# Performance work log

Hardware: AMD Instinct MI355X
Metric: run time of the kernel (lower is better)

The kernel has to match this reference:

```python
import jax, jax.numpy as jnp
import numpy as np

B, T, F, H = 64, 512, 512, 512  # batch, steps, features, hidden (both directions)


def setup_inputs() -> dict:
    key = jax.random.key(0)
    ks = jax.random.split(key, 7)
    s_in = 1.0 / np.sqrt(F)
    s_h = 1.0 / np.sqrt(H)
    return {
        "x": jax.random.normal(ks[0], (B, T, F), dtype=jnp.float32),
        "Wf": jax.random.normal(ks[1], (F, H), dtype=jnp.float32) * s_in,  # fw kernel
        "Uf": jax.random.normal(ks[2], (H, H), dtype=jnp.float32) * s_h,   # fw recurrent
        "bf": jnp.zeros((H,), dtype=jnp.float32),
        "Wb": jax.random.normal(ks[3], (F, H), dtype=jnp.float32) * s_in,  # bw kernel
        "Ub": jax.random.normal(ks[4], (H, H), dtype=jnp.float32) * s_h,   # bw recurrent
        "bb": jnp.zeros((H,), dtype=jnp.float32),
    }


def _rnn_scan(xs_tbf, W, U, b):
    # SimpleRNNCell: h' = tanh(x @ W + h @ U + b); xs_tbf: [T, B, F]
    h0 = jnp.zeros((xs_tbf.shape[1], U.shape[0]), dtype=xs_tbf.dtype)
    xw = jnp.einsum('tbf,fh->tbh', xs_tbf, W) + b  # precompute input projection

    def step(h, xw_t):
        h_new = jnp.tanh(xw_t + h @ U)
        return h_new, h_new

    _, ys = jax.lax.scan(step, h0, xw)  # ys: [T, B, H]
    return ys


def reference(x, Wf, Uf, bf, Wb, Ub, bb):
    xt = jnp.transpose(x, (1, 0, 2))              # [T, B, F]
    fw = _rnn_scan(xt, Wf, Uf, bf)                # time order
    bw = _rnn_scan(xt[::-1], Wb, Ub, bb)          # reverse-time order (NOT flipped back,
                                                  # matching the TF code which concats
                                                  # bw outputs in loop order)
    out = jnp.concatenate([fw, bw], axis=-1)      # [T, B, 2H]
    return jnp.transpose(out, (1, 0, 2))          # [B, T, 2H]
```

## Files before the change

### kernel.cpp

```cpp
#include <hip/hip_runtime.h>
#include <hip/hip_bf16.h>


using bf16 = __hip_bfloat16;
typedef __attribute__((ext_vector_type(8))) short short8;
typedef __attribute__((ext_vector_type(4))) float float4v;

#define T_STEPS 512

#define HB_OFF  1024
#define WS_ZERO_BYTES (HB_OFF + 2 * 131072 * 2)

__device__ __forceinline__ unsigned short f2bf(float f) {
    unsigned u = __builtin_bit_cast(unsigned, f);
    u = (u + 0x7fffu + ((u >> 16) & 1u)) >> 16;
    return (unsigned short)u;
}
__device__ __forceinline__ float bf2f(unsigned short s) {
    unsigned u = ((unsigned)s) << 16;
    return __builtin_bit_cast(float, u);
}

__global__ __launch_bounds__(256) void gemm_xw(
    const float* __restrict__ x,
    const float* __restrict__ Wf, const float* __restrict__ bf_,
    const float* __restrict__ Wb, const float* __restrict__ bb_,
    float* __restrict__ out)
{
    int bid = blockIdx.x;
    int dir = bid >> 12;
    int r   = bid & 4095;
    int i   = r & 63;
    int G   = r >> 6;
    int mt  = G * 8 + (i & 7);
    int nt  = i >> 3;
    const float* W    = dir ? Wb  : Wf;
    const float* bias = dir ? bb_ : bf_;

    __shared__ __align__(16) bf16 Xl[64][40];
    __shared__ __align__(16) bf16 Wt[64][40];

    int tid  = threadIdx.x;
    int wave = tid >> 6;
    int lane = tid & 63;
    int lm   = lane & 15;
    int quad = lane >> 4;

    float4v acc[4];
    #pragma unroll
    for (int q = 0; q < 4; ++q) acc[q] = (float4v){0.f, 0.f, 0.f, 0.f};

    int row0 = mt * 64;
    int srow = tid >> 2;
    int sk8  = (tid & 3) * 8;
    int wrow = tid >> 3;
    int wn8  = (tid & 7) * 8;

    for (int kt = 0; kt < 16; ++kt) {
        int k0 = kt * 32;
        const float* xp = x + (size_t)(row0 + srow) * 512 + k0 + sk8;
        float4v xa = *(const float4v*)xp;
        float4v xb = *(const float4v*)(xp + 4);
        union { short8 v; bf16 e[8]; } ux;
        ux.e[0] = __float2bfloat16(xa.x); ux.e[1] = __float2bfloat16(xa.y);
        ux.e[2] = __float2bfloat16(xa.z); ux.e[3] = __float2bfloat16(xa.w);
        ux.e[4] = __float2bfloat16(xb.x); ux.e[5] = __float2bfloat16(xb.y);
        ux.e[6] = __float2bfloat16(xb.z); ux.e[7] = __float2bfloat16(xb.w);
        *(short8*)&Xl[srow][sk8] = ux.v;
        const float* wp = W + (size_t)(k0 + wrow) * 512 + nt * 64 + wn8;
        float4v wa = *(const float4v*)wp;
        float4v wb = *(const float4v*)(wp + 4);
        Wt[wn8 + 0][wrow] = __float2bfloat16(wa.x);
        Wt[wn8 + 1][wrow] = __float2bfloat16(wa.y);
        Wt[wn8 + 2][wrow] = __float2bfloat16(wa.z);
        Wt[wn8 + 3][wrow] = __float2bfloat16(wa.w);
        Wt[wn8 + 4][wrow] = __float2bfloat16(wb.x);
        Wt[wn8 + 5][wrow] = __float2bfloat16(wb.y);
        Wt[wn8 + 6][wrow] = __float2bfloat16(wb.z);
        Wt[wn8 + 7][wrow] = __float2bfloat16(wb.w);
        __syncthreads();

        short8 a = *(const short8*)&Xl[wave * 16 + lm][quad * 8];
        #pragma unroll
        for (int n4 = 0; n4 < 4; ++n4) {
            short8 bfr = *(const short8*)&Wt[n4 * 16 + lm][quad * 8];
            acc[n4] = __builtin_amdgcn_mfma_f32_16x16x32_bf16(a, bfr, acc[n4], 0, 0, 0);
        }
        __syncthreads();
    }

    #pragma unroll
    for (int n4 = 0; n4 < 4; ++n4) {
        int ncol = nt * 64 + n4 * 16 + lm;
        float bv = bias[ncol];
        #pragma unroll
        for (int rr = 0; rr < 4; ++rr) {
            int m = wave * 16 + quad * 4 + rr;
            int gg = row0 + m;
            int b = gg >> 9;
            int t = gg & 511;
            int tp = dir ? (511 - t) : t;
            out[((size_t)b * T_STEPS + tp) * 1024 + dir * 512 + ncol] = acc[n4][rr] + bv;
        }
    }
}

__global__ __launch_bounds__(128, 1) void rnn_rec(
    const float* __restrict__ Uf, const float* __restrict__ Ub,
    float* __restrict__ out, unsigned char* __restrict__ ws)
{
    unsigned* flags = (unsigned*)ws;
    unsigned short* Hbuf = (unsigned short*)(ws + HB_OFF);

    int bid = blockIdx.x;
    int g   = bid & 31;
    int m   = bid >> 5;
    int n0  = g * 16;
    int m0  = m * 16;

    int tid  = threadIdx.x;
    int dir  = tid >> 6;
    int lane = tid & 63;
    int lm   = lane & 15;
    int quad = lane >> 4;

    const float* U = dir ? Ub : Uf;

    short8 Bh[16], Bl[16];
    #pragma unroll
    for (int kt = 0; kt < 16; ++kt) {
        union { short8 v; unsigned short e[8]; } h, l;
        #pragma unroll
        for (int j = 0; j < 8; ++j) {
            int k = kt * 32 + quad * 8 + j;
            float f = U[(size_t)k * 512 + n0 + lm];
            unsigned short hi = f2bf(f);
            h.e[j] = hi;
            l.e[j] = f2bf(f - bf2f(hi));
        }
        Bh[kt] = h.v;
        Bl[kt] = l.v;
    }

    unsigned* fbase = flags + (dir * 4 + m) * 32;
    unsigned short* base = Hbuf + (size_t)dir * 131072;
    float* od = out + (size_t)dir * 512;

    int rowb = m0 + quad * 4;
    int col  = n0 + lm;
    const size_t arow = (size_t)(m0 + lm) * 512;

    float xw[4];
    #pragma unroll
    for (int r = 0; r < 4; ++r)
        xw[r] = od[((size_t)(rowb + r) * T_STEPS + 0) * 1024 + col];

    for (int t = 0; t < T_STEPS; ++t) {
        int ph = t & 1;
        unsigned short* Hh = base + (size_t)ph * 65536;
        unsigned short* Hl = Hh + 32768;
        unsigned short* Wh = base + (size_t)(ph ^ 1) * 65536;
        unsigned short* Wl = Wh + 32768;

        if (t) {
            unsigned tgt = (unsigned)t;
            unsigned f;
            do {
                f = (lane < 32)
                  ? __hip_atomic_load(fbase + lane, __ATOMIC_RELAXED,
                                      __HIP_MEMORY_SCOPE_AGENT)
                  : tgt;
            } while (!__all(f >= tgt));
        }

        float4v aa = {0,0,0,0}, ab = {0,0,0,0}, ac = {0,0,0,0};
        #pragma unroll
        for (int kt = 0; kt < 16; ++kt) {
            int ko = kt * 32 + quad * 8;
            unsigned long long* pa = (unsigned long long*)(Hh + arow + ko);
            unsigned long long* pl = (unsigned long long*)(Hl + arow + ko);
            union { unsigned long long q[2]; short8 s; } ua, ul;
            ua.q[0] = __hip_atomic_load(pa,     __ATOMIC_RELAXED, __HIP_MEMORY_SCOPE_AGENT);
            ua.q[1] = __hip_atomic_load(pa + 1, __ATOMIC_RELAXED, __HIP_MEMORY_SCOPE_AGENT);
            ul.q[0] = __hip_atomic_load(pl,     __ATOMIC_RELAXED, __HIP_MEMORY_SCOPE_AGENT);
            ul.q[1] = __hip_atomic_load(pl + 1, __ATOMIC_RELAXED, __HIP_MEMORY_SCOPE_AGENT);
            aa = __builtin_amdgcn_mfma_f32_16x16x32_bf16(ua.s, Bh[kt], aa, 0, 0, 0);
            ab = __builtin_amdgcn_mfma_f32_16x16x32_bf16(ul.s, Bh[kt], ab, 0, 0, 0);
            ac = __builtin_amdgcn_mfma_f32_16x16x32_bf16(ua.s, Bl[kt], ac, 0, 0, 0);
        }

        float4v s = aa + ab + ac;
        float hv[4];
        #pragma unroll
        for (int r = 0; r < 4; ++r)
            hv[r] = tanhf(s[r] + xw[r]);

        #pragma unroll
        for (int r = 0; r < 4; ++r) {
            unsigned short hb = f2bf(hv[r]);
            unsigned short lb = f2bf(hv[r] - bf2f(hb));
            unsigned myw = (unsigned)hb | ((unsigned)lb << 16);
            unsigned p = (unsigned)__shfl_xor((int)myw, 1);
            if (!(lane & 1)) {
                unsigned hiw = (myw & 0xFFFFu) | (p << 16);
                unsigned low = (myw >> 16) | (p & 0xFFFF0000u);
                size_t off = (size_t)(rowb + r) * 512 + col;
                __hip_atomic_store((unsigned*)(Wh + off), hiw,
                                   __ATOMIC_RELAXED, __HIP_MEMORY_SCOPE_AGENT);
                __hip_atomic_store((unsigned*)(Wl + off), low,
                                   __ATOMIC_RELAXED, __HIP_MEMORY_SCOPE_AGENT);
            }
        }

        asm volatile("s_waitcnt vmcnt(0)" ::: "memory");
        if (lane == 0)
            __hip_atomic_store(fbase + g, (unsigned)(t + 1),
                               __ATOMIC_RELAXED, __HIP_MEMORY_SCOPE_AGENT);

        #pragma unroll
        for (int r = 0; r < 4; ++r)
            od[((size_t)(rowb + r) * T_STEPS + t) * 1024 + col] = hv[r];

        int tn = (t + 1 < T_STEPS) ? (t + 1) : t;
        #pragma unroll
        for (int r = 0; r < 4; ++r)
            xw[r] = od[((size_t)(rowb + r) * T_STEPS + tn) * 1024 + col];
    }
}

extern "C" void kernel_launch(void* const* d_in, const int* in_sizes, int n_in,
                              void* d_out, int out_size, void* d_ws, size_t ws_size,
                              hipStream_t stream) {
    const float* x   = (const float*)d_in[0];
    const float* Wf  = (const float*)d_in[1];
    const float* Uf  = (const float*)d_in[2];
    const float* bf_ = (const float*)d_in[3];
    const float* Wb  = (const float*)d_in[4];
    const float* Ub  = (const float*)d_in[5];
    const float* bb_ = (const float*)d_in[6];
    float* out = (float*)d_out;

    hipMemsetAsync(d_ws, 0, WS_ZERO_BYTES, stream);
    hipLaunchKernelGGL(gemm_xw, dim3(8192), dim3(256), 0, stream,
                       x, Wf, bf_, Wb, bb_, out);
    hipLaunchKernelGGL(rnn_rec, dim3(128), dim3(128), 0, stream,
                       Uf, Ub, out, (unsigned char*)d_ws);
}
```

Before: 4.253 ms.

## Co-locate recurrence groups per XCD and pipeline hidden-state loads with epoch flags

The recurrent kernel now assigns both waves of a block to the same direction and batch tile, so each group's 16 blocks are strided so they may land on one XCD. A startup barrier records each block's XCC id to decide whether a fast path is safe. The fast path polls flags with sc0 loads, which appear intended to stay coherent within an XCD, and software-pipelines the hidden-state loads with explicit vmcnt waits; otherwise it falls back to agent-scope atomics. Epoch-tagged flags, bumped by the GEMM kernel, avoid re-zeroing the large hidden buffer each call, the low part of U moves to LDS to save registers, and correctness now depends on the hardware's block placement and cache behaviour.

```diff
diff --git a/kernel.cpp b/kernel.cpp
--- a/kernel.cpp
+++ b/kernel.cpp
@@ -8,8 +8,8 @@
 
 #define T_STEPS 512
 
-#define HB_OFF  1024
-#define WS_ZERO_BYTES (HB_OFF + 2 * 131072 * 2)
+#define HB_OFF  2048
+#define WS_HDR_ZERO 1664
 
 __device__ __forceinline__ unsigned short f2bf(float f) {
     unsigned u = __builtin_bit_cast(unsigned, f);
@@ -25,9 +25,13 @@
     const float* __restrict__ x,
     const float* __restrict__ Wf, const float* __restrict__ bf_,
     const float* __restrict__ Wb, const float* __restrict__ bb_,
-    float* __restrict__ out)
+    float* __restrict__ out, unsigned char* __restrict__ ws)
 {
     int bid = blockIdx.x;
+    if (bid == 0 && threadIdx.x == 0) {
+        __hip_atomic_fetch_add((unsigned*)(ws + 1664), 1u,
+                               __ATOMIC_RELAXED, __HIP_MEMORY_SCOPE_AGENT);
+    }
     int dir = bid >> 12;
     int r   = bid & 4095;
     int i   = r & 63;
@@ -95,8 +99,8 @@
         float bv = bias[ncol];
         #pragma unroll
         for (int rr = 0; rr < 4; ++rr) {
-            int m = wave * 16 + quad * 4 + rr;
-            int gg = row0 + m;
+            int mm = wave * 16 + quad * 4 + rr;
+            int gg = row0 + mm;
             int b = gg >> 9;
             int t = gg & 511;
             int tp = dir ? (511 - t) : t;
@@ -110,39 +114,56 @@
     float* __restrict__ out, unsigned char* __restrict__ ws)
 {
     unsigned* flags = (unsigned*)ws;
+    unsigned* xcct  = (unsigned*)(ws + 1024);
+    unsigned* barc  = (unsigned*)(ws + 1536);
     unsigned short* Hbuf = (unsigned short*)(ws + HB_OFF);
 
     int bid = blockIdx.x;
-    int g   = bid & 31;
-    int m   = bid >> 5;
-    int n0  = g * 16;
-    int m0  = m * 16;
+    int grp = bid & 7;
+    int dir = grp >> 2;
+    int m   = grp & 3;
+    int j   = bid >> 3;
 
     int tid  = threadIdx.x;
-    int dir  = tid >> 6;
+    int wv   = tid >> 6;
     int lane = tid & 63;
     int lm   = lane & 15;
     int quad = lane >> 4;
+    int g    = j * 2 + wv;
+    int n0   = g * 16;
+    int m0   = m * 16;
+
+    unsigned ep = __hip_atomic_load((unsigned*)(ws + 1664),
+                                    __ATOMIC_RELAXED, __HIP_MEMORY_SCOPE_AGENT);
+    unsigned ebase = ep << 10;
+
+    if (tid == 0) {
+        unsigned xid = __builtin_amdgcn_s_getreg(20 | (0 << 6) | (31 << 11)) & 0xffu;
+        __hip_atomic_store(xcct + bid, xid | 0x100u,
+                           __ATOMIC_RELAXED, __HIP_MEMORY_SCOPE_AGENT);
+        __hip_atomic_fetch_add(barc, 1u, __ATOMIC_RELAXED, __HIP_MEMORY_SCOPE_AGENT);
+    }
 
     const float* U = dir ? Ub : Uf;
 
-    short8 Bh[16], Bl[16];
+    __shared__ __align__(16) short8 BlLds[2][16][64];
+    short8 Bh[16];
     #pragma unroll
     for (int kt = 0; kt < 16; ++kt) {
         union { short8 v; unsigned short e[8]; } h, l;
         #pragma unroll
-        for (int j = 0; j < 8; ++j) {
-            int k = kt * 32 + quad * 8 + j;
+        for (int jj = 0; jj < 8; ++jj) {
+            int k = kt * 32 + quad * 8 + jj;
             float f = U[(size_t)k * 512 + n0 + lm];
             unsigned short hi = f2bf(f);
-            h.e[j] = hi;
-            l.e[j] = f2bf(f - bf2f(hi));
+            h.e[jj] = hi;
+            l.e[jj] = f2bf(f - bf2f(hi));
         }
         Bh[kt] = h.v;
-        Bl[kt] = l.v;
-    }
-
-    unsigned* fbase = flags + (dir * 4 + m) * 32;
+        BlLds[wv][kt][lane] = l.v;
+    }
+
+    unsigned* fbase = flags + grp * 32;
     unsigned short* base = Hbuf + (size_t)dir * 131072;
     float* od = out + (size_t)dir * 512;
 
@@ -150,10 +171,30 @@
     int col  = n0 + lm;
     const size_t arow = (size_t)(m0 + lm) * 512;
 
-    float xw[4];
+    float xwl[4];
     #pragma unroll
     for (int r = 0; r < 4; ++r)
-        xw[r] = od[((size_t)(rowb + r) * T_STEPS + 0) * 1024 + col];
+        xwl[r] = od[((size_t)(rowb + r) * T_STEPS + 0) * 1024 + col];
+
+    if (tid == 0) {
+        while (__hip_atomic_load(barc, __ATOMIC_RELAXED,
+                                 __HIP_MEMORY_SCOPE_AGENT) < 128u)
+            __builtin_amdgcn_s_sleep(2);
+    }
+    __syncthreads();
+
+    unsigned e = (lane < 16)
+        ? __hip_atomic_load(xcct + grp + 8 * (lane & 15),
+                            __ATOMIC_RELAXED, __HIP_MEMORY_SCOPE_AGENT)
+        : 0u;
+    unsigned e0 = (unsigned)__shfl((int)e, 0);
+    bool same = __all((lane < 16) ? (e == e0) : 1);
+    unsigned eo = (lane == 0)
+        ? __hip_atomic_load(xcct + ((grp + 1) & 7),
+                            __ATOMIC_RELAXED, __HIP_MEMORY_SCOPE_AGENT)
+        : 0u;
+    eo = (unsigned)__shfl((int)eo, 0);
+    bool safe_mode = !(same && (eo != e0));
 
     for (int t = 0; t < T_STEPS; ++t) {
         int ph = t & 1;
@@ -162,38 +203,101 @@
         unsigned short* Wh = base + (size_t)(ph ^ 1) * 65536;
         unsigned short* Wl = Wh + 32768;
 
+        float4v aa = {0,0,0,0}, ab = {0,0,0,0}, ac = {0,0,0,0};
+
         if (t) {
-            unsigned tgt = (unsigned)t;
-            unsigned f;
-            do {
-                f = (lane < 32)
-                  ? __hip_atomic_load(fbase + lane, __ATOMIC_RELAXED,
-                                      __HIP_MEMORY_SCOPE_AGENT)
-                  : tgt;
-            } while (!__all(f >= tgt));
-        }
-
-        float4v aa = {0,0,0,0}, ab = {0,0,0,0}, ac = {0,0,0,0};
-        #pragma unroll
-        for (int kt = 0; kt < 16; ++kt) {
-            int ko = kt * 32 + quad * 8;
-            unsigned long long* pa = (unsigned long long*)(Hh + arow + ko);
-            unsigned long long* pl = (unsigned long long*)(Hl + arow + ko);
-            union { unsigned long long q[2]; short8 s; } ua, ul;
-            ua.q[0] = __hip_atomic_load(pa,     __ATOMIC_RELAXED, __HIP_MEMORY_SCOPE_AGENT);
-            ua.q[1] = __hip_atomic_load(pa + 1, __ATOMIC_RELAXED, __HIP_MEMORY_SCOPE_AGENT);
-            ul.q[0] = __hip_atomic_load(pl,     __ATOMIC_RELAXED, __HIP_MEMORY_SCOPE_AGENT);
-            ul.q[1] = __hip_atomic_load(pl + 1, __ATOMIC_RELAXED, __HIP_MEMORY_SCOPE_AGENT);
-            aa = __builtin_amdgcn_mfma_f32_16x16x32_bf16(ua.s, Bh[kt], aa, 0, 0, 0);
-            ab = __builtin_amdgcn_mfma_f32_16x16x32_bf16(ul.s, Bh[kt], ab, 0, 0, 0);
-            ac = __builtin_amdgcn_mfma_f32_16x16x32_bf16(ua.s, Bl[kt], ac, 0, 0, 0);
+            unsigned tgt = ebase + (unsigned)t;
+
+            if (!safe_mode) {
+                const unsigned* fp = fbase + (lane & 31);
+                unsigned fv;
+                bool ok = false;
+                int spins = 0;
+                do {
+                    asm volatile(
+                        "global_load_dword %0, %1, off sc0\n\t"
+                        "s_waitcnt vmcnt(0)"
+                        : "=v"(fv) : "v"(fp) : "memory");
+                    __builtin_amdgcn_sched_barrier(0);
+                    ok = __all((fv - tgt) < 1024u);
+                } while (!ok && ++spins < 128);
+                if (!ok) safe_mode = true;
+            }
+            if (safe_mode) {
+                unsigned fv;
+                do {
+                    fv = (lane < 32)
+                       ? __hip_atomic_load(fbase + lane, __ATOMIC_RELAXED,
+                                           __HIP_MEMORY_SCOPE_AGENT)
+                       : tgt;
+                } while (!__all((fv - tgt) < 1024u));
+            }
+
+            if (!safe_mode) {
+                asm volatile("s_waitcnt vmcnt(0)" ::: "memory");
+                short8 ha[3][4], la[3][4];
+                auto issueq = [&](int q, int buf) {
+                    #pragma unroll
+                    for (int i = 0; i < 4; ++i) {
+                        int kt = q * 4 + i;
+                        const unsigned short* pa = Hh + arow + kt * 32 + quad * 8;
+                        const unsigned short* pl = Hl + arow + kt * 32 + quad * 8;
+                        asm volatile("global_load_dwordx4 %0, %1, off sc0"
+                                     : "=v"(ha[buf][i]) : "v"(pa) : "memory");
+                        asm volatile("global_load_dwordx4 %0, %1, off sc0"
+                                     : "=v"(la[buf][i]) : "v"(pl) : "memory");
+                    }
+                };
+                auto compq = [&](int q, int buf) {
+                    short8 blv[4];
+                    #pragma unroll
+                    for (int i = 0; i < 4; ++i)
+                        blv[i] = BlLds[wv][q * 4 + i][lane];
+                    #pragma unroll
+                    for (int i = 0; i < 4; ++i) {
+                        int kt = q * 4 + i;
+                        aa = __builtin_amdgcn_mfma_f32_16x16x32_bf16(ha[buf][i], Bh[kt], aa, 0, 0, 0);
+                        ab = __builtin_amdgcn_mfma_f32_16x16x32_bf16(la[buf][i], Bh[kt], ab, 0, 0, 0);
+                        ac = __builtin_amdgcn_mfma_f32_16x16x32_bf16(ha[buf][i], blv[i], ac, 0, 0, 0);
+                    }
+                };
+                issueq(0, 0); issueq(1, 1);
+                asm volatile("s_waitcnt vmcnt(8)" ::: "memory");
+                __builtin_amdgcn_sched_barrier(0);
+                compq(0, 0); issueq(2, 2);
+                asm volatile("s_waitcnt vmcnt(8)" ::: "memory");
+                __builtin_amdgcn_sched_barrier(0);
+                compq(1, 1); issueq(3, 0);
+                asm volatile("s_waitcnt vmcnt(8)" ::: "memory");
+                __builtin_amdgcn_sched_barrier(0);
+                compq(2, 2);
+                asm volatile("s_waitcnt vmcnt(0)" ::: "memory");
+                __builtin_amdgcn_sched_barrier(0);
+                compq(3, 0);
+            } else {
+                #pragma unroll
+                for (int kt = 0; kt < 16; ++kt) {
+                    int ko = kt * 32 + quad * 8;
+                    unsigned long long* pa = (unsigned long long*)(Hh + arow + ko);
+                    unsigned long long* pl = (unsigned long long*)(Hl + arow + ko);
+                    union { unsigned long long q[2]; short8 s; } ua, ul;
+                    ua.q[0] = __hip_atomic_load(pa,     __ATOMIC_RELAXED, __HIP_MEMORY_SCOPE_AGENT);
+                    ua.q[1] = __hip_atomic_load(pa + 1, __ATOMIC_RELAXED, __HIP_MEMORY_SCOPE_AGENT);
+                    ul.q[0] = __hip_atomic_load(pl,     __ATOMIC_RELAXED, __HIP_MEMORY_SCOPE_AGENT);
+                    ul.q[1] = __hip_atomic_load(pl + 1, __ATOMIC_RELAXED, __HIP_MEMORY_SCOPE_AGENT);
+                    short8 blv = BlLds[wv][kt][lane];
+                    aa = __builtin_amdgcn_mfma_f32_16x16x32_bf16(ua.s, Bh[kt], aa, 0, 0, 0);
+                    ab = __builtin_amdgcn_mfma_f32_16x16x32_bf16(ul.s, Bh[kt], ab, 0, 0, 0);
+                    ac = __builtin_amdgcn_mfma_f32_16x16x32_bf16(ua.s, blv,    ac, 0, 0, 0);
+                }
+            }
         }
 
         float4v s = aa + ab + ac;
         float hv[4];
         #pragma unroll
         for (int r = 0; r < 4; ++r)
-            hv[r] = tanhf(s[r] + xw[r]);
+            hv[r] = tanhf(s[r] + xwl[r]);
 
         #pragma unroll
         for (int r = 0; r < 4; ++r) {
@@ -214,7 +318,7 @@
 
         asm volatile("s_waitcnt vmcnt(0)" ::: "memory");
         if (lane == 0)
-            __hip_atomic_store(fbase + g, (unsigned)(t + 1),
+            __hip_atomic_store(fbase + g, ebase + (unsigned)(t + 1),
                                __ATOMIC_RELAXED, __HIP_MEMORY_SCOPE_AGENT);
 
         #pragma unroll
@@ -224,7 +328,7 @@
         int tn = (t + 1 < T_STEPS) ? (t + 1) : t;
         #pragma unroll
         for (int r = 0; r < 4; ++r)
-            xw[r] = od[((size_t)(rowb + r) * T_STEPS + tn) * 1024 + col];
+            xwl[r] = od[((size_t)(rowb + r) * T_STEPS + tn) * 1024 + col];
     }
 }
 
@@ -240,9 +344,9 @@
     const float* bb_ = (const float*)d_in[6];
     float* out = (float*)d_out;
 
-    hipMemsetAsync(d_ws, 0, WS_ZERO_BYTES, stream);
+    hipMemsetAsync(d_ws, 0, WS_HDR_ZERO, stream);
     hipLaunchKernelGGL(gemm_xw, dim3(8192), dim3(256), 0, stream,
-                       x, Wf, bf_, Wb, bb_, out);
+                       x, Wf, bf_, Wb, bb_, out, (unsigned char*)d_ws);
     hipLaunchKernelGGL(rnn_rec, dim3(128), dim3(128), 0, stream,
                        Uf, Ub, out, (unsigned char*)d_ws);
 }
```

Measured after the change: 3.774 ms. -11.2%, faster.
